# Kernel tuning notes

Hardware: AMD Instinct MI355X
Metric: run time of the kernel (lower is better)

Reference implementation:

```python
import jax, jax.numpy as jnp
import numpy as np

D, NH, NL, NP, NLAYERS = 256, 8, 4, 4, 6
DH = D // NH
SHAPES = [(76, 100), (38, 50), (19, 25), (10, 13)]
STARTS = [int(s) for s in np.cumsum([0] + [h * w for h, w in SHAPES])[:-1]]
LQ = sum(h * w for h, w in SHAPES)
B = 2


def _layernorm(x, g, b, eps=1e-5):
    m = x.mean(-1, keepdims=True)
    v = ((x - m) ** 2).mean(-1, keepdims=True)
    return (x - m) * jax.lax.rsqrt(v + eps) * g + b


def _ref_points():
    pts = []
    for H, W in SHAPES:
        ry = (jnp.arange(H, dtype=jnp.float32) + 0.5) / H
        rx = (jnp.arange(W, dtype=jnp.float32) + 0.5) / W
        gy, gx = jnp.meshgrid(ry, rx, indexing='ij')
        pts.append(jnp.stack([gx.ravel(), gy.ravel()], -1))
    ref = jnp.concatenate(pts, 0)  # [LQ, 2] (x, y)
    return jnp.broadcast_to(ref[:, None, :], (LQ, NL, 2))


def _bilinear(v, loc, H, W):
    # v: [BN, H*W, DH]; loc: [BN, N, 2] normalized (x, y).
    # Matches torch grid_sample(align_corners=False, padding='zeros') with grid=2*loc-1.
    px = loc[..., 0] * W - 0.5
    py = loc[..., 1] * H - 0.5
    x0f = jnp.floor(px)
    y0f = jnp.floor(py)
    lx = px - x0f
    ly = py - y0f
    x0 = x0f.astype(jnp.int32)
    y0 = y0f.astype(jnp.int32)
    out = jnp.zeros(loc.shape[:-1] + (DH,), v.dtype)
    for dy, dx, w in ((0, 0, (1 - ly) * (1 - lx)), (0, 1, (1 - ly) * lx), (1, 0, ly * (1 - lx)), (1, 1, ly * lx)):
        xi = x0 + dx
        yi = y0 + dy
        valid = (xi >= 0) & (xi < W) & (yi >= 0) & (yi < H)
        idx = jnp.clip(yi, 0, H - 1) * W + jnp.clip(xi, 0, W - 1)
        g = jnp.take_along_axis(v, idx[..., None], axis=1)  # [BN, N, DH]
        out = out + g * (w * valid)[..., None]
    return out


def _layer(src, pos, ref, p):
    q = src + pos
    value = (src @ p['w_val'] + p['b_val']).reshape(B, LQ, NH, DH)
    off = (q @ p['w_off'] + p['b_off']).reshape(B, LQ, NH, NL, NP, 2)
    aw = jax.nn.softmax((q @ p['w_attn'] + p['b_attn']).reshape(B, LQ, NH, NL * NP), -1)
    aw = aw.reshape(B, LQ, NH, NL, NP)
    norm = jnp.array([[w, h] for h, w in SHAPES], jnp.float32)  # [NL, 2] = (W, H)
    loc = ref[None, :, None, :, None, :] + off / norm[None, None, None, :, None, :]  # [B,LQ,NH,NL,NP,2]
    v_t = value.transpose(0, 2, 1, 3).reshape(B * NH, LQ, DH)
    out = jnp.zeros((B, NH, LQ, DH), src.dtype)
    for l, (H, W) in enumerate(SHAPES):
        vl = v_t[:, STARTS[l]:STARTS[l] + H * W]
        locl = loc[:, :, :, l].transpose(0, 2, 1, 3, 4).reshape(B * NH, LQ * NP, 2)
        g = _bilinear(vl, locl, H, W).reshape(B, NH, LQ, NP, DH)
        out = out + jnp.einsum('bhqp,bhqpd->bhqd', aw[:, :, :, l].transpose(0, 2, 1, 3), g)
    attn = out.transpose(0, 2, 1, 3).reshape(B, LQ, D) @ p['w_out'] + p['b_out']
    src = _layernorm(src + attn, p['ln1_g'], p['ln1_b'])
    ffn = jax.nn.relu(src @ p['w_ffn1'] + p['b_ffn1']) @ p['w_ffn2'] + p['b_ffn2']
    return _layernorm(src + ffn, p['ln2_g'], p['ln2_b'])


def setup_inputs() -> dict:
    key = jax.random.key(0)
    ks = jax.random.split(key, 16)
    inp = {}
    for i, (H, W) in enumerate(SHAPES):
        inp[f'src{i}'] = jax.random.normal(ks[i], (B, D, H, W), jnp.float32)
        inp[f'pos{i}'] = jax.random.normal(ks[4 + i], (B, D, H, W), jnp.float32)
    inp['level_embed'] = jax.random.normal(ks[8], (NL, D), jnp.float32)
    s = 0.02
    inp['w_off'] = jax.random.normal(ks[9], (NLAYERS, D, NH * NL * NP * 2), jnp.float32) * s
    inp['b_off'] = jnp.zeros((NLAYERS, NH * NL * NP * 2), jnp.float32)
    inp['w_attn'] = jax.random.normal(ks[10], (NLAYERS, D, NH * NL * NP), jnp.float32) * s
    inp['b_attn'] = jnp.zeros((NLAYERS, NH * NL * NP), jnp.float32)
    inp['w_val'] = jax.random.normal(ks[11], (NLAYERS, D, D), jnp.float32) * s
    inp['b_val'] = jnp.zeros((NLAYERS, D), jnp.float32)
    inp['w_out'] = jax.random.normal(ks[12], (NLAYERS, D, D), jnp.float32) * s
    inp['b_out'] = jnp.zeros((NLAYERS, D), jnp.float32)
    inp['ln1_g'] = jnp.ones((NLAYERS, D), jnp.float32)
    inp['ln1_b'] = jnp.zeros((NLAYERS, D), jnp.float32)
    inp['w_ffn1'] = jax.random.normal(ks[13], (NLAYERS, D, 1024), jnp.float32) * s
    inp['b_ffn1'] = jnp.zeros((NLAYERS, 1024), jnp.float32)
    inp['w_ffn2'] = jax.random.normal(ks[14], (NLAYERS, 1024, D), jnp.float32) * s
    inp['b_ffn2'] = jnp.zeros((NLAYERS, D), jnp.float32)
    inp['ln2_g'] = jnp.ones((NLAYERS, D), jnp.float32)
    inp['ln2_b'] = jnp.zeros((NLAYERS, D), jnp.float32)
    return inp


def reference(src0, src1, src2, src3, pos0, pos1, pos2, pos3, level_embed,
              w_off, b_off, w_attn, b_attn, w_val, b_val, w_out, b_out,
              ln1_g, ln1_b, w_ffn1, b_ffn1, w_ffn2, b_ffn2, ln2_g, ln2_b):
    srcs = [src0, src1, src2, src3]
    poss = [pos0, pos1, pos2, pos3]
    src_flat = jnp.concatenate(
        [s.reshape(B, D, -1).transpose(0, 2, 1) + level_embed[l][None, None] for l, s in enumerate(srcs)], 1)
    pos_flat = jnp.concatenate([p.reshape(B, D, -1).transpose(0, 2, 1) for p in poss], 1)
    ref = _ref_points()
    x = src_flat
    for i in range(NLAYERS):
        p = dict(w_off=w_off[i], b_off=b_off[i], w_attn=w_attn[i], b_attn=b_attn[i],
                 w_val=w_val[i], b_val=b_val[i], w_out=w_out[i], b_out=b_out[i],
                 ln1_g=ln1_g[i], ln1_b=ln1_b[i], w_ffn1=w_ffn1[i], b_ffn1=b_ffn1[i],
                 w_ffn2=w_ffn2[i], b_ffn2=b_ffn2[i], ln2_g=ln2_g[i], ln2_b=ln2_b[i])
        x = _layer(x, pos_flat, ref, p)
    return x  # [B, LQ, D] encoded memory
```

## Files before the change

kernel.cpp:

```cpp
#include <hip/hip_runtime.h>
#include <math.h>

#define LQ 10105
#define BATCH 2
#define NLAYERS 6
#define NTOK (BATCH * LQ)

typedef __attribute__((ext_vector_type(8))) short bf16x8;
typedef __attribute__((ext_vector_type(4))) float f32x4;

__device__ inline unsigned short f2bf_rne(float f) {
    unsigned u = __float_as_uint(f);
    unsigned r = u + 0x7fffu + ((u >> 16) & 1u);
    return (unsigned short)(r >> 16);
}
__device__ inline float bf2f(unsigned short h) {
    return __uint_as_float((unsigned)h << 16);
}
__device__ inline void split2(float v, unsigned short& h, unsigned short& l) {
    h = (unsigned short)(__float_as_uint(v) >> 16);
    float r = v - bf2f(h);
    l = (unsigned short)(__float_as_uint(r) >> 16);
}

__device__ inline void stage_plane(const unsigned short* __restrict__ gp,
                                   unsigned short* lp, int row0, int K, int kt,
                                   int tid)
{
    int r  = row0 + (tid >> 2);
    int kk = kt + (tid & 3) * 8;
    __builtin_amdgcn_global_load_lds(
        (const __attribute__((address_space(1))) void*)(gp + (size_t)r * K + kk),
        (__attribute__((address_space(3))) void*)(lp + tid * 8), 16, 0, 0);
    __builtin_amdgcn_global_load_lds(
        (const __attribute__((address_space(1))) void*)(gp + (size_t)(r + 64) * K + kk),
        (__attribute__((address_space(3))) void*)(lp + 2048 + tid * 8), 16, 0, 0);
}

__global__ __launch_bounds__(256)
void flatten_k(const float* __restrict__ src, const float* __restrict__ pos,
               const float* __restrict__ lvl, float* __restrict__ srcf,
               float* __restrict__ posf, unsigned short* __restrict__ sh,
               unsigned short* __restrict__ sl, unsigned short* __restrict__ qh,
               unsigned short* __restrict__ ql, int HW, int start)
{
    __shared__ float ts[64][65], tp[64][65];
    int hw0 = blockIdx.x * 64;
    int d0  = blockIdx.y * 64;
    int b   = blockIdx.z;
    int tid = threadIdx.x;
    int c = tid & 63, rg = tid >> 6;

    #pragma unroll 4
    for (int i = 0; i < 16; ++i) {
        int dl = rg * 16 + i;
        int hw = hw0 + c;
        float s = 0.f, p = 0.f;
        if (hw < HW) {
            s = src[(size_t)(b * 256 + d0 + dl) * HW + hw];
            p = pos[(size_t)(b * 256 + d0 + dl) * HW + hw];
        }
        ts[dl][c] = s;
        tp[dl][c] = p;
    }
    __syncthreads();
    float lv = lvl[d0 + c];
    #pragma unroll 4
    for (int i = 0; i < 16; ++i) {
        int hwl = rg * 16 + i;
        int hw = hw0 + hwl;
        if (hw >= HW) continue;
        float s = ts[c][hwl] + lv;
        float p = tp[c][hwl];
        size_t o = (size_t)(b * LQ + start + hw) * 256 + d0 + c;
        srcf[o] = s;
        posf[o] = p;
        unsigned short h, l;
        split2(s, h, l); sh[o] = h; sl[o] = l;
        float q = s + p;
        split2(q, h, l); qh[o] = h; ql[o] = l;
    }
}

__global__ __launch_bounds__(256)
void wsplit_k(const float* __restrict__ W, unsigned short* __restrict__ Th,
              unsigned short* __restrict__ Tl, int K, int N,
              long srcStride, long dstStride)
{
    __shared__ float t[32][33];
    int layer = blockIdx.z;
    int n0 = blockIdx.x * 32, k0 = blockIdx.y * 32;
    int tx = threadIdx.x & 31, ty = threadIdx.x >> 5;
    const float* Wsrc = W + (size_t)layer * srcStride;
    #pragma unroll
    for (int i = 0; i < 4; ++i)
        t[ty + i * 8][tx] = Wsrc[(size_t)(k0 + ty + i * 8) * N + n0 + tx];
    __syncthreads();
    unsigned short* th = Th + (size_t)layer * dstStride;
    unsigned short* tl = Tl + (size_t)layer * dstStride;
    #pragma unroll
    for (int i = 0; i < 4; ++i) {
        int n = n0 + ty + i * 8;
        float v = t[tx][ty + i * 8];
        unsigned short h = f2bf_rne(v);
        th[(size_t)n * K + k0 + tx] = h;
        tl[(size_t)n * K + k0 + tx] = f2bf_rne(v - bf2f(h));
    }
}

__global__ void boa_k(const float* __restrict__ b_val,
                      const float* __restrict__ b_off,
                      const float* __restrict__ b_attn, float* __restrict__ bo)
{
    int l = blockIdx.x, t = threadIdx.x;
    float v;
    if (t < 256)      v = b_val[l * 256 + t];
    else if (t < 512) v = b_off[l * 256 + (t - 256)];
    else              v = b_attn[l * 128 + (t - 512)];
    bo[l * 640 + t] = v;
}

__global__ __launch_bounds__(256)
void gemm_top(const unsigned short* __restrict__ Ash,
              const unsigned short* __restrict__ Asl,
              const unsigned short* __restrict__ Aqh,
              const unsigned short* __restrict__ Aql,
              const unsigned short* __restrict__ Bh,
              const unsigned short* __restrict__ Bl,
              const float* __restrict__ bias640,
              unsigned short* __restrict__ valb, float* __restrict__ oab, int M)
{
    constexpr int K = 256, NB = 5;
    __shared__ unsigned short sP[4 * 4096];
    unsigned short* sAh = sP;
    unsigned short* sAl = sP + 4096;
    unsigned short* sBh = sP + 8192;
    unsigned short* sBl = sP + 12288;

    const int nwg = gridDim.x, bid = blockIdx.x;
    const int q8 = nwg >> 3, r8 = nwg & 7, xcd = bid & 7;
    const int work = (xcd < r8 ? xcd * (q8 + 1) : r8 * (q8 + 1) + (xcd - r8) * q8)
                     + (bid >> 3);
    const int mblk = work / NB;
    const int nb = work - mblk * NB;
    const int m0 = mblk * 128, n0 = nb * 128;

    const unsigned short* Ah = (nb < 2) ? Ash : Aqh;
    const unsigned short* Al = (nb < 2) ? Asl : Aql;

    const int tid = threadIdx.x;
    const int w = tid >> 6, l = tid & 63;
    const int wm = (w >> 1) * 64, wn = (w & 1) * 64;
    const int lr = l & 15, kb = (l >> 4) * 8, rr = (l >> 4) * 4;

    f32x4 acc[4][4];
    #pragma unroll
    for (int i = 0; i < 4; ++i)
        #pragma unroll
        for (int j = 0; j < 4; ++j) acc[i][j] = (f32x4){0.f, 0.f, 0.f, 0.f};

    for (int kt = 0; kt < K; kt += 32) {
        stage_plane(Ah, sAh, m0, K, kt, tid);
        stage_plane(Al, sAl, m0, K, kt, tid);
        stage_plane(Bh, sBh, n0, K, kt, tid);
        stage_plane(Bl, sBl, n0, K, kt, tid);
        __syncthreads();
        bf16x8 fah[4], fal[4];
        #pragma unroll
        for (int mf = 0; mf < 4; ++mf) {
            int off = (wm + mf * 16 + lr) * 32 + kb;
            fah[mf] = *(const bf16x8*)&sAh[off];
            fal[mf] = *(const bf16x8*)&sAl[off];
        }
        #pragma unroll
        for (int nf = 0; nf < 4; ++nf) {
            int boff = (wn + nf * 16 + lr) * 32 + kb;
            bf16x8 fbh = *(const bf16x8*)&sBh[boff];
            bf16x8 fbl = *(const bf16x8*)&sBl[boff];
            #pragma unroll
            for (int mf = 0; mf < 4; ++mf) {
                f32x4 c = acc[mf][nf];
                c = __builtin_amdgcn_mfma_f32_16x16x32_bf16(fah[mf], fbh, c, 0, 0, 0);
                c = __builtin_amdgcn_mfma_f32_16x16x32_bf16(fah[mf], fbl, c, 0, 0, 0);
                c = __builtin_amdgcn_mfma_f32_16x16x32_bf16(fal[mf], fbh, c, 0, 0, 0);
                acc[mf][nf] = c;
            }
        }
        __syncthreads();
    }

    #pragma unroll
    for (int nf = 0; nf < 4; ++nf) {
        int ncol = n0 + wn + nf * 16 + lr;
        float bs = bias640[ncol];
        #pragma unroll
        for (int mf = 0; mf < 4; ++mf) {
            int rowb = m0 + wm + mf * 16 + rr;
            #pragma unroll
            for (int r = 0; r < 4; ++r) {
                int row = rowb + r;
                if (row < M) {
                    float v = acc[mf][nf][r] + bs;
                    if (nb < 2) valb[(size_t)row * 256 + ncol] = f2bf_rne(v);
                    else        oab[(size_t)row * 384 + (ncol - 256)] = v;
                }
            }
        }
    }
}

template<int PASSES, bool RELU, bool HAS_RES, bool C_BF16>
__global__ __launch_bounds__(256)
void gemm_std(const unsigned short* __restrict__ Ah,
              const unsigned short* __restrict__ Al,
              const unsigned short* __restrict__ Bh,
              const unsigned short* __restrict__ Bl,
              const float* __restrict__ bias, const float* __restrict__ Res,
              void* __restrict__ Cv, int M, int N, int K, int NB)
{
    __shared__ unsigned short sP[(PASSES + 1) * 4096];
    unsigned short* sAh = sP;
    unsigned short* sAl = sP + 4096;
    unsigned short* sBh = sP + (PASSES - 1) * 4096;
    unsigned short* sBl = sP + PASSES * 4096;

    const int nwg = gridDim.x, bid = blockIdx.x;
    const int q8 = nwg >> 3, r8 = nwg & 7, xcd = bid & 7;
    const int work = (xcd < r8 ? xcd * (q8 + 1) : r8 * (q8 + 1) + (xcd - r8) * q8)
                     + (bid >> 3);
    const int mblk = work / NB;
    const int m0 = mblk * 128;
    const int n0 = (work - mblk * NB) * 128;

    const int tid = threadIdx.x;
    const int w = tid >> 6, l = tid & 63;
    const int wm = (w >> 1) * 64, wn = (w & 1) * 64;
    const int lr = l & 15, kb = (l >> 4) * 8, rr = (l >> 4) * 4;

    f32x4 acc[4][4];
    #pragma unroll
    for (int i = 0; i < 4; ++i)
        #pragma unroll
        for (int j = 0; j < 4; ++j) acc[i][j] = (f32x4){0.f, 0.f, 0.f, 0.f};

    for (int kt = 0; kt < K; kt += 32) {
        stage_plane(Ah, sAh, m0, K, kt, tid);
        if (PASSES == 3) stage_plane(Al, sAl, m0, K, kt, tid);
        stage_plane(Bh, sBh, n0, K, kt, tid);
        stage_plane(Bl, sBl, n0, K, kt, tid);
        __syncthreads();
        bf16x8 fah[4], fal[4];
        #pragma unroll
        for (int mf = 0; mf < 4; ++mf) {
            int off = (wm + mf * 16 + lr) * 32 + kb;
            fah[mf] = *(const bf16x8*)&sAh[off];
            if (PASSES == 3) fal[mf] = *(const bf16x8*)&sAl[off];
        }
        #pragma unroll
        for (int nf = 0; nf < 4; ++nf) {
            int boff = (wn + nf * 16 + lr) * 32 + kb;
            bf16x8 fbh = *(const bf16x8*)&sBh[boff];
            bf16x8 fbl = *(const bf16x8*)&sBl[boff];
            #pragma unroll
            for (int mf = 0; mf < 4; ++mf) {
                f32x4 c = acc[mf][nf];
                c = __builtin_amdgcn_mfma_f32_16x16x32_bf16(fah[mf], fbh, c, 0, 0, 0);
                c = __builtin_amdgcn_mfma_f32_16x16x32_bf16(fah[mf], fbl, c, 0, 0, 0);
                if (PASSES == 3)
                    c = __builtin_amdgcn_mfma_f32_16x16x32_bf16(fal[mf], fbh, c, 0, 0, 0);
                acc[mf][nf] = c;
            }
        }
        __syncthreads();
    }

    float* Cf = (float*)Cv;
    unsigned short* Cb = (unsigned short*)Cv;
    #pragma unroll
    for (int nf = 0; nf < 4; ++nf) {
        int ncol = n0 + wn + nf * 16 + lr;
        float bs = bias[ncol];
        #pragma unroll
        for (int mf = 0; mf < 4; ++mf) {
            int rowb = m0 + wm + mf * 16 + rr;
            #pragma unroll
            for (int r = 0; r < 4; ++r) {
                int row = rowb + r;
                if (row < M) {
                    float v = acc[mf][nf][r] + bs;
                    if (HAS_RES) v += Res[(size_t)row * N + ncol];
                    if (RELU) v = fmaxf(v, 0.f);
                    if (C_BF16) Cb[(size_t)row * N + ncol] = f2bf_rne(v);
                    else        Cf[(size_t)row * N + ncol] = v;
                }
            }
        }
    }
}

__global__ __launch_bounds__(256)
void sample_k(const unsigned short* __restrict__ val,
              const float* __restrict__ oab, unsigned short* __restrict__ out)
{
    const int Hs[4] = {76, 38, 19, 10};
    const int Ws[4] = {100, 50, 25, 13};
    const int ST[4] = {0, 7600, 9500, 9975};

    int bid = blockIdx.x;
    int xcd = bid & 7;
    const int qch = LQ >> 3;
    const int rem = LQ & 7;
    int q = (xcd < rem ? xcd * (qch + 1) : rem * (qch + 1) + (xcd - rem) * qch)
            + (bid >> 3);
    int b = blockIdx.y;
    int tid = threadIdx.x;

    __shared__ int2 s_iw[512];

    if (tid < 128) {
        int h = tid >> 4, pt = tid & 15, lvl = pt >> 2, p = pt & 3;
        int lq, local;
        if (q < 7600)      { lq = 0; local = q; }
        else if (q < 9500) { lq = 1; local = q - 7600; }
        else if (q < 9975) { lq = 2; local = q - 9500; }
        else               { lq = 3; local = q - 9975; }
        int Wq = Ws[lq], Hq = Hs[lq];
        int ry = local / Wq, rx = local - ry * Wq;
        float refx = (rx + 0.5f) / (float)Wq;
        float refy = (ry + 0.5f) / (float)Hq;

        size_t rowb = (size_t)(b * LQ + q) * 384;
        float logit = oab[rowb + 256 + h * 16 + pt];
        float mx = logit;
        mx = fmaxf(mx, __shfl_xor(mx, 1, 64));
        mx = fmaxf(mx, __shfl_xor(mx, 2, 64));
        mx = fmaxf(mx, __shfl_xor(mx, 4, 64));
        mx = fmaxf(mx, __shfl_xor(mx, 8, 64));
        float e = expf(logit - mx);
        float s = e;
        s += __shfl_xor(s, 1, 64);
        s += __shfl_xor(s, 2, 64);
        s += __shfl_xor(s, 4, 64);
        s += __shfl_xor(s, 8, 64);
        float aw = e / s;

        float ox = oab[rowb + h * 32 + lvl * 8 + p * 2];
        float oy = oab[rowb + h * 32 + lvl * 8 + p * 2 + 1];
        int W = Ws[lvl], H = Hs[lvl], st = ST[lvl];
        float px = refx * (float)W + ox - 0.5f;
        float py = refy * (float)H + oy - 0.5f;
        float x0f = floorf(px), y0f = floorf(py);
        float lx = px - x0f, ly = py - y0f;
        int x0 = (int)x0f, y0 = (int)y0f;
        int x1 = x0 + 1, y1 = y0 + 1;
        float ax0 = ((x0 >= 0) & (x0 < W)) ? (1.f - lx) : 0.f;
        float ax1 = ((x1 >= 0) & (x1 < W)) ? lx : 0.f;
        float ay0 = ((y0 >= 0) & (y0 < H)) ? (1.f - ly) : 0.f;
        float ay1 = ((y1 >= 0) & (y1 < H)) ? ly : 0.f;
        int cx0 = min(max(x0, 0), W - 1), cx1 = min(max(x1, 0), W - 1);
        int cy0 = min(max(y0, 0), H - 1), cy1 = min(max(y1, 0), H - 1);
        int i00 = st + cy0 * W + cx0, i01 = st + cy0 * W + cx1;
        int i10 = st + cy1 * W + cx0, i11 = st + cy1 * W + cx1;
        int base4 = tid * 4;
        s_iw[base4 + 0] = make_int2(i00, __float_as_int(aw * ay0 * ax0));
        s_iw[base4 + 1] = make_int2(i01, __float_as_int(aw * ay0 * ax1));
        s_iw[base4 + 2] = make_int2(i10, __float_as_int(aw * ay1 * ax0));
        s_iw[base4 + 3] = make_int2(i11, __float_as_int(aw * ay1 * ax1));
    }
    __syncthreads();

    int lane   = tid & 63;
    int wv     = tid >> 6;
    int h      = wv * 2 + (lane >> 5);
    int half   = lane & 31;
    int corner = half >> 3;
    int c4     = half & 7;
    const unsigned short* vb = val + (size_t)(b * LQ) * 256 + h * 32 + c4 * 4;
    int sbase = h * 64 + corner;

    float4 acc = make_float4(0.f, 0.f, 0.f, 0.f);
    #pragma unroll
    for (int pt = 0; pt < 16; ++pt) {
        int2 iw = s_iw[sbase + pt * 4];
        float wgt = __int_as_float(iw.y);
        ushort4 v = *(const ushort4*)&vb[(size_t)iw.x * 256];
        acc.x += wgt * bf2f(v.x); acc.y += wgt * bf2f(v.y);
        acc.z += wgt * bf2f(v.z); acc.w += wgt * bf2f(v.w);
    }
    acc.x += __shfl_xor(acc.x, 8, 64);  acc.y += __shfl_xor(acc.y, 8, 64);
    acc.z += __shfl_xor(acc.z, 8, 64);  acc.w += __shfl_xor(acc.w, 8, 64);
    acc.x += __shfl_xor(acc.x, 16, 64); acc.y += __shfl_xor(acc.y, 16, 64);
    acc.z += __shfl_xor(acc.z, 16, 64); acc.w += __shfl_xor(acc.w, 16, 64);

    if (corner == 0) {
        ushort4 o;
        o.x = f2bf_rne(acc.x); o.y = f2bf_rne(acc.y);
        o.z = f2bf_rne(acc.z); o.w = f2bf_rne(acc.w);
        *(ushort4*)&out[(size_t)(b * LQ + q) * 256 + h * 32 + c4 * 4] = o;
    }
}

template<bool EMIT_Q, bool EMIT_PLANES>
__global__ __launch_bounds__(256)
void ln_plane_k(const float* __restrict__ x, const float* __restrict__ g,
                const float* __restrict__ bt, const float* __restrict__ pos,
                float* __restrict__ dst, unsigned short* __restrict__ sh,
                unsigned short* __restrict__ sl, unsigned short* __restrict__ qh,
                unsigned short* __restrict__ ql, int nrows)
{
    int row = blockIdx.x * 4 + (threadIdx.x >> 6);
    int lane = threadIdx.x & 63;
    if (row >= nrows) return;

    float4 v = *(const float4*)&x[(size_t)row * 256 + lane * 4];
    float s = v.x + v.y + v.z + v.w;
    #pragma unroll
    for (int o = 32; o > 0; o >>= 1) s += __shfl_down(s, o, 64);
    s = __shfl(s, 0, 64);
    float m = s * (1.0f / 256.0f);
    float cx = v.x - m, cy = v.y - m, cz = v.z - m, cw = v.w - m;
    float s2 = cx * cx + cy * cy + cz * cz + cw * cw;
    #pragma unroll
    for (int o = 32; o > 0; o >>= 1) s2 += __shfl_down(s2, o, 64);
    s2 = __shfl(s2, 0, 64);
    float rstd = rsqrtf(s2 * (1.0f / 256.0f) + 1e-5f);

    float4 gv = *(const float4*)&g[lane * 4];
    float4 bv = *(const float4*)&bt[lane * 4];
    float4 r;
    r.x = cx * rstd * gv.x + bv.x;
    r.y = cy * rstd * gv.y + bv.y;
    r.z = cz * rstd * gv.z + bv.z;
    r.w = cw * rstd * gv.w + bv.w;
    size_t o4 = (size_t)row * 256 + lane * 4;
    *(float4*)&dst[o4] = r;

    if (EMIT_PLANES) {
        ushort4 hh, ll;
        split2(r.x, hh.x, ll.x); split2(r.y, hh.y, ll.y);
        split2(r.z, hh.z, ll.z); split2(r.w, hh.w, ll.w);
        *(ushort4*)&sh[o4] = hh;
        *(ushort4*)&sl[o4] = ll;
    }
    if (EMIT_Q) {
        float4 pv = *(const float4*)&pos[o4];
        ushort4 hh, ll;
        split2(r.x + pv.x, hh.x, ll.x); split2(r.y + pv.y, hh.y, ll.y);
        split2(r.z + pv.z, hh.z, ll.z); split2(r.w + pv.w, hh.w, ll.w);
        *(ushort4*)&qh[o4] = hh;
        *(ushort4*)&ql[o4] = ll;
    }
}

extern "C" void kernel_launch(void* const* d_in, const int* in_sizes, int n_in,
                              void* d_out, int out_size, void* d_ws, size_t ws_size,
                              hipStream_t stream)
{
    const float* src_in[4] = {(const float*)d_in[0], (const float*)d_in[2],
                              (const float*)d_in[4], (const float*)d_in[6]};
    const float* pos_in[4] = {(const float*)d_in[1], (const float*)d_in[3],
                              (const float*)d_in[5], (const float*)d_in[7]};
    const float* lvl    = (const float*)d_in[8];
    const float* w_off  = (const float*)d_in[9];
    const float* b_off  = (const float*)d_in[10];
    const float* w_attn = (const float*)d_in[11];
    const float* b_attn = (const float*)d_in[12];
    const float* w_val  = (const float*)d_in[13];
    const float* b_val  = (const float*)d_in[14];
    const float* w_out  = (const float*)d_in[15];
    const float* b_out  = (const float*)d_in[16];
    const float* ln1_g  = (const float*)d_in[17];
    const float* ln1_b  = (const float*)d_in[18];
    const float* w_ffn1 = (const float*)d_in[19];
    const float* b_ffn1 = (const float*)d_in[20];
    const float* w_ffn2 = (const float*)d_in[21];
    const float* b_ffn2 = (const float*)d_in[22];
    const float* ln2_g  = (const float*)d_in[23];
    const float* ln2_b  = (const float*)d_in[24];

    char* wsb = (char*)d_ws;
    float* src  = (float*)wsb;
    float* pos  = src + (size_t)NTOK * 256;
    float* preln = pos + (size_t)NTOK * 256;
    unsigned short* sh = (unsigned short*)(preln + (size_t)NTOK * 256);
    unsigned short* sl = sh + (size_t)NTOK * 256;
    unsigned short* qh = sl + (size_t)NTOK * 256;
    unsigned short* ql = qh + (size_t)NTOK * 256;
    char* uni = (char*)(ql + (size_t)NTOK * 256);
    unsigned short* valb = (unsigned short*)uni;
    float* oab = (float*)(uni + (size_t)NTOK * 512);
    unsigned short* samp = (unsigned short*)(uni + (size_t)NTOK * 2048);
    unsigned short* ffnb = (unsigned short*)uni;
    float* boa640 = (float*)(uni + (size_t)NTOK * 2560);
    unsigned short* Wh = (unsigned short*)(boa640 + 6 * 640);
    const long WL = 753664;
    unsigned short* Wl = Wh + (size_t)NLAYERS * WL;
    const long O_VAL = 0, O_OFF = 65536, O_ATT = 131072, O_OUT = 163840,
               O_F1 = 229376, O_F2 = 491520;

    wsplit_k<<<dim3(8, 8, 6),  256, 0, stream>>>(w_val,  Wh + O_VAL, Wl + O_VAL, 256, 256,  65536, WL);
    wsplit_k<<<dim3(8, 8, 6),  256, 0, stream>>>(w_off,  Wh + O_OFF, Wl + O_OFF, 256, 256,  65536, WL);
    wsplit_k<<<dim3(4, 8, 6),  256, 0, stream>>>(w_attn, Wh + O_ATT, Wl + O_ATT, 256, 128,  32768, WL);
    wsplit_k<<<dim3(8, 8, 6),  256, 0, stream>>>(w_out,  Wh + O_OUT, Wl + O_OUT, 256, 256,  65536, WL);
    wsplit_k<<<dim3(32, 8, 6), 256, 0, stream>>>(w_ffn1, Wh + O_F1,  Wl + O_F1,  256, 1024, 262144, WL);
    wsplit_k<<<dim3(8, 32, 6), 256, 0, stream>>>(w_ffn2, Wh + O_F2,  Wl + O_F2,  1024, 256, 262144, WL);
    boa_k<<<dim3(6), dim3(640), 0, stream>>>(b_val, b_off, b_attn, boa640);

    const int HWs[4] = {7600, 1900, 475, 130};
    const int STt[4] = {0, 7600, 9500, 9975};
    for (int l = 0; l < 4; ++l) {
        dim3 g((HWs[l] + 63) / 64, 4, BATCH);
        flatten_k<<<g, 256, 0, stream>>>(src_in[l], pos_in[l], lvl + l * 256,
                                         src, pos, sh, sl, qh, ql, HWs[l], STt[l]);
    }

    const int MB = (NTOK + 127) / 128;
    const int LNB = (NTOK + 3) / 4;
    dim3 blk(256);

    for (int i = 0; i < NLAYERS; ++i) {
        const unsigned short* whL = Wh + (size_t)i * WL;
        const unsigned short* wlL = Wl + (size_t)i * WL;
        const float* bou = b_out  + (size_t)i * 256;
        const float* l1g = ln1_g  + (size_t)i * 256;
        const float* l1b = ln1_b  + (size_t)i * 256;
        const float* bf1 = b_ffn1 + (size_t)i * 1024;
        const float* bf2 = b_ffn2 + (size_t)i * 256;
        const float* l2g = ln2_g  + (size_t)i * 256;
        const float* l2b = ln2_b  + (size_t)i * 256;

        gemm_top<<<dim3(MB * 5), blk, 0, stream>>>(
            sh, sl, qh, ql, whL, wlL, boa640 + (size_t)i * 640, valb, oab, NTOK);
        sample_k<<<dim3(LQ, BATCH), blk, 0, stream>>>(valb, oab, samp);
        gemm_std<2, false, true, false><<<dim3(MB * 2), blk, 0, stream>>>(
            samp, nullptr, whL + O_OUT, wlL + O_OUT, bou, src, preln,
            NTOK, 256, 256, 2);
        ln_plane_k<false, true><<<dim3(LNB), blk, 0, stream>>>(
            preln, l1g, l1b, nullptr, src, sh, sl, nullptr, nullptr, NTOK);
        gemm_std<3, true, false, true><<<dim3(MB * 8), blk, 0, stream>>>(
            sh, sl, whL + O_F1, wlL + O_F1, bf1, nullptr, ffnb,
            NTOK, 1024, 256, 8);
        gemm_std<2, false, true, false><<<dim3(MB * 2), blk, 0, stream>>>(
            ffnb, nullptr, whL + O_F2, wlL + O_F2, bf2, src, preln,
            NTOK, 256, 1024, 2);
        if (i == NLAYERS - 1)
            ln_plane_k<false, false><<<dim3(LNB), blk, 0, stream>>>(
                preln, l2g, l2b, nullptr, (float*)d_out,
                nullptr, nullptr, nullptr, nullptr, NTOK);
        else
            ln_plane_k<true, true><<<dim3(LNB), blk, 0, stream>>>(
                preln, l2g, l2b, pos, src, sh, sl, qh, ql, NTOK);
    }
}
```

Measured before the change: 1.792 ms.

## Double-buffer LDS staging and XOR-swizzle tiles in split-bf16 GEMMs

Both GEMM kernels now keep two LDS buffers, so the global-to-LDS load of the next K slice overlaps the MFMA compute on the current one. The loop is unrolled by two with one barrier per half-step. Staging now XOR-swizzles the 16-byte chunk slot by row, and the fragment reads apply the matching swizzle, to reduce LDS bank conflicts. LDS use per block doubles, which may lower occupancy. The loop also assumes K is a multiple of 64.

```diff
diff --git a/kernel.cpp b/kernel.cpp
--- a/kernel.cpp
+++ b/kernel.cpp
@@ -27,13 +27,14 @@
                                    unsigned short* lp, int row0, int K, int kt,
                                    int tid)
 {
-    int r  = row0 + (tid >> 2);
-    int kk = kt + (tid & 3) * 8;
+    int rloc = tid >> 2;
+    int slot = (tid & 3) ^ ((tid >> 3) & 3);
+    int kk   = kt + slot * 8;
     __builtin_amdgcn_global_load_lds(
-        (const __attribute__((address_space(1))) void*)(gp + (size_t)r * K + kk),
+        (const __attribute__((address_space(1))) void*)(gp + (size_t)(row0 + rloc) * K + kk),
         (__attribute__((address_space(3))) void*)(lp + tid * 8), 16, 0, 0);
     __builtin_amdgcn_global_load_lds(
-        (const __attribute__((address_space(1))) void*)(gp + (size_t)(r + 64) * K + kk),
+        (const __attribute__((address_space(1))) void*)(gp + (size_t)(row0 + rloc + 64) * K + kk),
         (__attribute__((address_space(3))) void*)(lp + 2048 + tid * 8), 16, 0, 0);
 }
 
@@ -131,11 +132,7 @@
               unsigned short* __restrict__ valb, float* __restrict__ oab, int M)
 {
     constexpr int K = 256, NB = 5;
-    __shared__ unsigned short sP[4 * 4096];
-    unsigned short* sAh = sP;
-    unsigned short* sAl = sP + 4096;
-    unsigned short* sBh = sP + 8192;
-    unsigned short* sBl = sP + 12288;
+    __shared__ unsigned short sP[2 * 4 * 4096];
 
     const int nwg = gridDim.x, bid = blockIdx.x;
     const int q8 = nwg >> 3, r8 = nwg & 7, xcd = bid & 7;
@@ -151,7 +148,8 @@
     const int tid = threadIdx.x;
     const int w = tid >> 6, l = tid & 63;
     const int wm = (w >> 1) * 64, wn = (w & 1) * 64;
-    const int lr = l & 15, kb = (l >> 4) * 8, rr = (l >> 4) * 4;
+    const int lr = l & 15, rr = (l >> 4) * 4;
+    const int so = (((l >> 4) ^ ((lr >> 1) & 3)) * 8);
 
     f32x4 acc[4][4];
     #pragma unroll
@@ -159,24 +157,27 @@
         #pragma unroll
         for (int j = 0; j < 4; ++j) acc[i][j] = (f32x4){0.f, 0.f, 0.f, 0.f};
 
-    for (int kt = 0; kt < K; kt += 32) {
-        stage_plane(Ah, sAh, m0, K, kt, tid);
-        stage_plane(Al, sAl, m0, K, kt, tid);
-        stage_plane(Bh, sBh, n0, K, kt, tid);
-        stage_plane(Bl, sBl, n0, K, kt, tid);
-        __syncthreads();
+    auto STAGE = [&](int b, int kt) {
+        unsigned short* base = sP + b * 16384;
+        stage_plane(Ah, base,         m0, K, kt, tid);
+        stage_plane(Al, base + 4096,  m0, K, kt, tid);
+        stage_plane(Bh, base + 8192,  n0, K, kt, tid);
+        stage_plane(Bl, base + 12288, n0, K, kt, tid);
+    };
+    auto COMPUTE = [&](int b) {
+        unsigned short* base = sP + b * 16384;
         bf16x8 fah[4], fal[4];
         #pragma unroll
         for (int mf = 0; mf < 4; ++mf) {
-            int off = (wm + mf * 16 + lr) * 32 + kb;
-            fah[mf] = *(const bf16x8*)&sAh[off];
-            fal[mf] = *(const bf16x8*)&sAl[off];
+            int off = (wm + mf * 16 + lr) * 32 + so;
+            fah[mf] = *(const bf16x8*)&base[off];
+            fal[mf] = *(const bf16x8*)&base[4096 + off];
         }
         #pragma unroll
         for (int nf = 0; nf < 4; ++nf) {
-            int boff = (wn + nf * 16 + lr) * 32 + kb;
-            bf16x8 fbh = *(const bf16x8*)&sBh[boff];
-            bf16x8 fbl = *(const bf16x8*)&sBl[boff];
+            int boff = (wn + nf * 16 + lr) * 32 + so;
+            bf16x8 fbh = *(const bf16x8*)&base[8192 + boff];
+            bf16x8 fbl = *(const bf16x8*)&base[12288 + boff];
             #pragma unroll
             for (int mf = 0; mf < 4; ++mf) {
                 f32x4 c = acc[mf][nf];
@@ -186,6 +187,16 @@
                 acc[mf][nf] = c;
             }
         }
+    };
+
+    STAGE(0, 0);
+    __syncthreads();
+    for (int kt = 0; kt < K; kt += 64) {
+        STAGE(1, kt + 32);
+        COMPUTE(0);
+        __syncthreads();
+        if (kt + 64 < K) STAGE(0, kt + 64);
+        COMPUTE(1);
         __syncthreads();
     }
 
@@ -218,11 +229,8 @@
               const float* __restrict__ bias, const float* __restrict__ Res,
               void* __restrict__ Cv, int M, int N, int K, int NB)
 {
-    __shared__ unsigned short sP[(PASSES + 1) * 4096];
-    unsigned short* sAh = sP;
-    unsigned short* sAl = sP + 4096;
-    unsigned short* sBh = sP + (PASSES - 1) * 4096;
-    unsigned short* sBl = sP + PASSES * 4096;
+    constexpr int NPL = PASSES + 1;
+    __shared__ unsigned short sP[2 * NPL * 4096];
 
     const int nwg = gridDim.x, bid = blockIdx.x;
     const int q8 = nwg >> 3, r8 = nwg & 7, xcd = bid & 7;
@@ -235,7 +243,8 @@
     const int tid = threadIdx.x;
     const int w = tid >> 6, l = tid & 63;
     const int wm = (w >> 1) * 64, wn = (w & 1) * 64;
-    const int lr = l & 15, kb = (l >> 4) * 8, rr = (l >> 4) * 4;
+    const int lr = l & 15, rr = (l >> 4) * 4;
+    const int so = (((l >> 4) ^ ((lr >> 1) & 3)) * 8);
 
     f32x4 acc[4][4];
     #pragma unroll
@@ -243,24 +252,27 @@
         #pragma unroll
         for (int j = 0; j < 4; ++j) acc[i][j] = (f32x4){0.f, 0.f, 0.f, 0.f};
 
-    for (int kt = 0; kt < K; kt += 32) {
-        stage_plane(Ah, sAh, m0, K, kt, tid);
-        if (PASSES == 3) stage_plane(Al, sAl, m0, K, kt, tid);
-        stage_plane(Bh, sBh, n0, K, kt, tid);
-        stage_plane(Bl, sBl, n0, K, kt, tid);
-        __syncthreads();
+    auto STAGE = [&](int b, int kt) {
+        unsigned short* base = sP + b * (NPL * 4096);
+        stage_plane(Ah, base, m0, K, kt, tid);
+        if (PASSES == 3) stage_plane(Al, base + 4096, m0, K, kt, tid);
+        stage_plane(Bh, base + (PASSES - 1) * 4096, n0, K, kt, tid);
+        stage_plane(Bl, base + PASSES * 4096, n0, K, kt, tid);
+    };
+    auto COMPUTE = [&](int b) {
+        unsigned short* base = sP + b * (NPL * 4096);
         bf16x8 fah[4], fal[4];
         #pragma unroll
         for (int mf = 0; mf < 4; ++mf) {
-            int off = (wm + mf * 16 + lr) * 32 + kb;
-            fah[mf] = *(const bf16x8*)&sAh[off];
-            if (PASSES == 3) fal[mf] = *(const bf16x8*)&sAl[off];
+            int off = (wm + mf * 16 + lr) * 32 + so;
+            fah[mf] = *(const bf16x8*)&base[off];
+            if (PASSES == 3) fal[mf] = *(const bf16x8*)&base[4096 + off];
         }
         #pragma unroll
         for (int nf = 0; nf < 4; ++nf) {
-            int boff = (wn + nf * 16 + lr) * 32 + kb;
-            bf16x8 fbh = *(const bf16x8*)&sBh[boff];
-            bf16x8 fbl = *(const bf16x8*)&sBl[boff];
+            int boff = (wn + nf * 16 + lr) * 32 + so;
+            bf16x8 fbh = *(const bf16x8*)&base[(PASSES - 1) * 4096 + boff];
+            bf16x8 fbl = *(const bf16x8*)&base[PASSES * 4096 + boff];
             #pragma unroll
             for (int mf = 0; mf < 4; ++mf) {
                 f32x4 c = acc[mf][nf];
@@ -271,6 +283,16 @@
                 acc[mf][nf] = c;
             }
         }
+    };
+
+    STAGE(0, 0);
+    __syncthreads();
+    for (int kt = 0; kt < K; kt += 64) {
+        STAGE(1, kt + 32);
+        COMPUTE(0);
+        __syncthreads();
+        if (kt + 64 < K) STAGE(0, kt + 64);
+        COMPUTE(1);
         __syncthreads();
     }
 
```

Result: faster. 1.719 ms (-4.1%).
